# Kernel tuning notes

Measured on AMD Instinct MI355X. Metric: run time of the kernel, lower is better.

The kernel has to match this reference:

```python
import jax, jax.numpy as jnp
import numpy as np

B, H, W, C = 32, 256, 256, 3
FLAT = (H // 4) * (W // 4) * 64  # 64*64*64 = 262144 after two stride-2 SAME convs


def _conv(x, k, b, stride):
    y = jax.lax.conv_general_dilated(
        x, k, (stride, stride), 'SAME',
        dimension_numbers=('NHWC', 'HWIO', 'NHWC'))
    return jax.nn.relu(y + b)


def _grid_sample(img, theta):
    # STN: build normalized affine grid from theta [B,2,3], bilinear sample with
    # zero padding for out-of-bounds (GridSampler2D semantics).
    b, h, w, c = img.shape
    xs = (2.0 * jnp.arange(w, dtype=img.dtype) + 1.0) / w - 1.0
    ys = (2.0 * jnp.arange(h, dtype=img.dtype) + 1.0) / h - 1.0
    X, Y = jnp.meshgrid(xs, ys)                      # [H,W]
    base = jnp.stack([X, Y, jnp.ones_like(X)], -1)   # [H,W,3]
    g = jnp.einsum('bij,hwj->bhwi', theta, base)     # [B,H,W,2] (x,y) in [-1,1]
    px = (g[..., 0] + 1.0) * 0.5 * w - 0.5
    py = (g[..., 1] + 1.0) * 0.5 * h - 0.5
    x0 = jnp.floor(px); y0 = jnp.floor(py)
    wx1 = px - x0; wx0 = 1.0 - wx1
    wy1 = py - y0; wy0 = 1.0 - wy1

    bidx = jnp.arange(b)[:, None, None]

    def gather(yi, xi):
        valid = (xi >= 0) & (xi < w) & (yi >= 0) & (yi < h)
        xc = jnp.clip(xi, 0, w - 1).astype(jnp.int32)
        yc = jnp.clip(yi, 0, h - 1).astype(jnp.int32)
        v = img[bidx, yc, xc]                        # [B,H,W,C]
        return v * valid[..., None].astype(img.dtype)

    out = (gather(y0, x0) * (wy0 * wx0)[..., None]
           + gather(y0, x0 + 1) * (wy0 * wx1)[..., None]
           + gather(y0 + 1, x0) * (wy1 * wx0)[..., None]
           + gather(y0 + 1, x0 + 1) * (wy1 * wx1)[..., None])
    return out


def setup_inputs() -> dict:
    key = jax.random.key(0)
    ks = jax.random.split(key, 9)
    s = 0.05
    return {
        'inputs': jax.random.uniform(ks[0], (B, H, W, C), jnp.float32),
        'k1': jax.random.normal(ks[1], (3, 3, C, 32), jnp.float32) * s,
        'b1': jnp.zeros((32,), jnp.float32),
        'k2': jax.random.normal(ks[2], (3, 3, 32, 64), jnp.float32) * s,
        'b2': jnp.zeros((64,), jnp.float32),
        'w1': jax.random.normal(ks[3], (FLAT, 128), jnp.float32) * 0.002,
        'd1': jnp.zeros((128,), jnp.float32),
        'w2': jax.random.normal(ks[4], (128, 6), jnp.float32) * s,
        'd2': jnp.asarray([1, 0, 0, 0, 1, 0], jnp.float32),  # identity-ish bias
    }


def reference(inputs, k1, b1, k2, b2, w1, d1, w2, d2):
    x = _conv(inputs, k1, b1, 2)          # [B,H/2,W/2,32]
    x = _conv(x, k2, b2, 2)               # [B,H/4,W/4,64]
    x = x.reshape(x.shape[0], -1)         # [B,FLAT]
    x = jax.nn.relu(x @ w1 + d1)          # [B,128]
    theta = (x @ w2 + d2).reshape(-1, 2, 3)
    return _grid_sample(inputs, theta)
```

## Files before the change

### kernel.cpp

```cpp
#include <hip/hip_runtime.h>

#define IN_H 256
#define IN_W 256
#define C0   3
#define C1   32
#define H1   128
#define C2   64
#define H2   64
#define NB   32
#define K_FLAT (H2*H2*C2)
#define NHID 128

#define A1_IDX(b,p,y,ci,x2) ((((((size_t)(b)*2 + (p))*H1 + (y))*C1 + (ci))*64) + (x2))

__global__ __launch_bounds__(256, 8)
void conv1_k(const float* __restrict__ in, const float* __restrict__ k1,
             const float* __restrict__ b1, float* __restrict__ a1p) {
  __shared__ __align__(16) float rowL[3*IN_W*C0];
  const int tid = threadIdx.x;
  const int oy  = blockIdx.x;
  const int b   = blockIdx.y;

  {
    const float4* src = (const float4*)(in + (size_t)(b*IN_H + 2*oy)*IN_W*C0);
    float4* dst = (float4*)rowL;
    const float4 z = make_float4(0.f,0.f,0.f,0.f);
#pragma unroll
    for (int j = 0; j < 3; ++j) {
      const int i = tid + j*256;
      if (i < 3*IN_W*C0/4) {
        const int row = i / (IN_W*C0/4);
        const bool ok = (2*oy + row) < IN_H;
        dst[i] = ok ? src[i] : z;
      }
    }
  }
  __syncthreads();

  const int ox  = tid & 127;
  const int cg  = __builtin_amdgcn_readfirstlane((tid >> 7) * 16);

  float acc[16];
#pragma unroll
  for (int co = 0; co < 16; ++co) acc[co] = b1[cg + co];

#pragma unroll
  for (int dy = 0; dy < 3; ++dy) {
#pragma unroll
    for (int dx = 0; dx < 3; ++dx) {
      const int ix  = 2*ox + dx;
      const bool ok = ix < IN_W;
      const float m  = ok ? 1.f : 0.f;
      const int ixc = ok ? ix : (IN_W-1);
      const float* lp = rowL + (dy*IN_W + ixc)*C0;
      const float v0 = lp[0] * m;
      const float v1 = lp[1] * m;
      const float v2 = lp[2] * m;
      const float* wp = k1 + (size_t)((dy*3+dx)*C0)*C1 + cg;
#pragma unroll
      for (int co = 0; co < 16; ++co)
        acc[co] = fmaf(v0, wp[co],
                  fmaf(v1, wp[C1+co],
                  fmaf(v2, wp[2*C1+co], acc[co])));
    }
  }
  const int p  = ox & 1;
  const int x2 = ox >> 1;
#pragma unroll
  for (int co = 0; co < 16; ++co)
    a1p[A1_IDX(b, p, oy, cg + co, x2)] = fmaxf(acc[co], 0.f);
}

#define CONV2_DY_LOOP(EDGE_)                                                   \
  _Pragma("unroll")                                                            \
  for (int dy = 0; dy < 3; ++dy) {                                             \
    int iy = 2*oy + dy;                                                        \
    float rm = 1.f;                                                            \
    if (EDGE_) { if (iy >= H1) { iy = H1 - 1; rm = 0.f; } }                    \
    const float* r0 = a1p + A1_IDX(b, 0, iy, 0, 0) + 2*lx;                     \
    const float* r1 = a1p + A1_IDX(b, 1, iy, 0, 0) + 2*lx;                     \
    const float* wp = k2 + (size_t)(dy*3*C1)*C2 + cg16;                        \
    const float m2 = EDGE_ ? rm * xm : xm;                                     \
    _Pragma("unroll 8")                                                        \
    for (int ci = 0; ci < C1; ++ci) {                                          \
      const float2 Av = *(const float2*)(r0 + (size_t)ci*64);                  \
      const float  A2 = r0[(size_t)ci*64 + 2];                                 \
      const float2 Bv = *(const float2*)(r1 + (size_t)ci*64);                  \
      const float ax = EDGE_ ? Av.x*rm : Av.x;                                 \
      const float ay = EDGE_ ? Av.y*rm : Av.y;                                 \
      const float bx = EDGE_ ? Bv.x*rm : Bv.x;                                 \
      const float by = EDGE_ ? Bv.y*rm : Bv.y;                                 \
      const float a2v = A2 * m2;                                               \
      const float* w0  = wp + (size_t)ci*C2;                                   \
      const float* w1r = wp + (size_t)(C1 + ci)*C2;                            \
      const float* w2r = wp + (size_t)(2*C1 + ci)*C2;                          \
      _Pragma("unroll")                                                        \
      for (int co = 0; co < 16; ++co) {                                        \
        acc0[co] = fmaf(ax, w0[co],                                            \
                   fmaf(bx, w1r[co],                                           \
                   fmaf(ay,  w2r[co], acc0[co])));                             \
        acc1[co] = fmaf(ay, w0[co],                                            \
                   fmaf(by, w1r[co],                                           \
                   fmaf(a2v, w2r[co], acc1[co])));                             \
      }                                                                        \
    }                                                                          \
  }

__global__ __launch_bounds__(256, 4)
void conv2_k(const float* __restrict__ a1p, const float* __restrict__ k2,
             const float* __restrict__ b2, float* __restrict__ a2) {
  const int tid  = threadIdx.x;
  const int lane = tid & 63;
  const int lx   = lane & 31;
  const int oys  = lane >> 5;
  const int cg16 = __builtin_amdgcn_readfirstlane((tid >> 6) * 16);
  const int oy   = blockIdx.x * 2 + oys;
  const int b    = blockIdx.y;

  float acc0[16], acc1[16];
#pragma unroll
  for (int co = 0; co < 16; ++co) { acc0[co] = b2[cg16 + co]; acc1[co] = acc0[co]; }

  const float xm = (lx == 31) ? 0.f : 1.f;

  if (blockIdx.x == 31) {
    CONV2_DY_LOOP(1)
  } else {
    CONV2_DY_LOOP(0)
  }

  float* op = a2 + ((size_t)((b*H2 + oy)*H2) + 2*lx)*C2 + cg16;
#pragma unroll
  for (int g = 0; g < 4; ++g) {
    float4 o0;
    o0.x = fmaxf(acc0[4*g+0], 0.f);
    o0.y = fmaxf(acc0[4*g+1], 0.f);
    o0.z = fmaxf(acc0[4*g+2], 0.f);
    o0.w = fmaxf(acc0[4*g+3], 0.f);
    ((float4*)op)[g] = o0;
    float4 o1;
    o1.x = fmaxf(acc1[4*g+0], 0.f);
    o1.y = fmaxf(acc1[4*g+1], 0.f);
    o1.z = fmaxf(acc1[4*g+2], 0.f);
    o1.w = fmaxf(acc1[4*g+3], 0.f);
    ((float4*)(op + C2))[g] = o1;
  }
}

#define FC1_G   2048
#define KSPAN   (K_FLAT / FC1_G)
#define SUB     64
#define GC1     16

__global__ __launch_bounds__(256, 3)
void fc1_partial_k(const float* __restrict__ a2, const float* __restrict__ w1,
                   float* __restrict__ partial) {
  __shared__ __align__(16) float wL[SUB*NHID];
  __shared__ __align__(16) float xT[SUB*36];
  const int tid = threadIdx.x;
  const int q   = tid & 31;
  const int bo  = tid >> 5;
  const int k0  = blockIdx.x * KSPAN;

  float4 a0 = make_float4(0.f,0.f,0.f,0.f), a1v = a0, a2v = a0, a3v = a0;

#pragma unroll
  for (int r = 0; r < KSPAN/SUB; ++r) {
    const int ks = k0 + r*SUB;
    if (r) __syncthreads();

    {
      const float4* wsrc = (const float4*)(w1 + (size_t)ks*NHID);
#pragma unroll
      for (int j = 0; j < 8; ++j)
        ((float4*)wL)[tid + j*256] = wsrc[tid + j*256];
    }
    {
      const int lb  = tid >> 3;
      const int lkq = tid & 7;
#pragma unroll
      for (int j = 0; j < 2; ++j) {
        const int k4 = lkq*4 + j*32;
        float4 t = *(const float4*)(a2 + (size_t)lb*K_FLAT + ks + k4);
        xT[(k4+0)*36 + lb] = t.x;
        xT[(k4+1)*36 + lb] = t.y;
        xT[(k4+2)*36 + lb] = t.z;
        xT[(k4+3)*36 + lb] = t.w;
      }
    }
    __syncthreads();

#pragma unroll 8
    for (int k = 0; k < SUB; ++k) {
      const float4 w4 = *(const float4*)(wL + k*NHID + 4*q);
      const float4 xb = *(const float4*)&xT[k*36 + 4*bo];
      a0.x = fmaf(xb.x, w4.x, a0.x); a0.y = fmaf(xb.x, w4.y, a0.y);
      a0.z = fmaf(xb.x, w4.z, a0.z); a0.w = fmaf(xb.x, w4.w, a0.w);
      a1v.x = fmaf(xb.y, w4.x, a1v.x); a1v.y = fmaf(xb.y, w4.y, a1v.y);
      a1v.z = fmaf(xb.y, w4.z, a1v.z); a1v.w = fmaf(xb.y, w4.w, a1v.w);
      a2v.x = fmaf(xb.z, w4.x, a2v.x); a2v.y = fmaf(xb.z, w4.y, a2v.y);
      a2v.z = fmaf(xb.z, w4.z, a2v.z); a2v.w = fmaf(xb.z, w4.w, a2v.w);
      a3v.x = fmaf(xb.w, w4.x, a3v.x); a3v.y = fmaf(xb.w, w4.y, a3v.y);
      a3v.z = fmaf(xb.w, w4.z, a3v.z); a3v.w = fmaf(xb.w, w4.w, a3v.w);
    }
  }

  float* pp = partial + (size_t)blockIdx.x*(NB*NHID) + 4*q;
  *(float4*)(pp + (4*bo+0)*NHID) = a0;
  *(float4*)(pp + (4*bo+1)*NHID) = a1v;
  *(float4*)(pp + (4*bo+2)*NHID) = a2v;
  *(float4*)(pp + (4*bo+3)*NHID) = a3v;
}

__global__ __launch_bounds__(128, 8)
void fc1_reduce1_k(const float* __restrict__ partial, float* __restrict__ partial2) {
  const int t  = blockIdx.x*128 + threadIdx.x;
  const int gc = blockIdx.y;
  float s = 0.f;
#pragma unroll 8
  for (int g = gc*(FC1_G/GC1); g < gc*(FC1_G/GC1) + (FC1_G/GC1); ++g)
    s += partial[(size_t)g*(NB*NHID) + t];
  partial2[(size_t)gc*(NB*NHID) + t] = s;
}

__global__ __launch_bounds__(256)
void fc1_reduce2_k(const float* __restrict__ partial2, const float* __restrict__ d1,
                   float* __restrict__ h) {
  const int t = blockIdx.x*256 + threadIdx.x;
  float s = 0.f;
#pragma unroll
  for (int gc = 0; gc < GC1; ++gc) s += partial2[(size_t)gc*(NB*NHID) + t];
  h[t] = fmaxf(s + d1[t & (NHID-1)], 0.f);
}

__global__ __launch_bounds__(192)
void theta_k(const float* __restrict__ h, const float* __restrict__ w2,
             const float* __restrict__ d2, float* __restrict__ theta) {
  const int t = threadIdx.x;
  if (t >= NB*6) return;
  const int b = t / 6, j = t % 6;
  float s0 = 0.f, s1 = 0.f, s2 = 0.f, s3 = 0.f;
  for (int n = 0; n < NHID; n += 4) {
    s0 = fmaf(h[b*NHID + n+0], w2[(n+0)*6 + j], s0);
    s1 = fmaf(h[b*NHID + n+1], w2[(n+1)*6 + j], s1);
    s2 = fmaf(h[b*NHID + n+2], w2[(n+2)*6 + j], s2);
    s3 = fmaf(h[b*NHID + n+3], w2[(n+3)*6 + j], s3);
  }
  theta[t] = (s0 + s1) + (s2 + s3) + d2[j];
}

__global__ __launch_bounds__(256)
void sample_k(const float* __restrict__ img, const float* __restrict__ theta,
              float* __restrict__ out) {
  const int x = threadIdx.x;
  const int y = blockIdx.x & (IN_H-1);
  const int b = blockIdx.x >> 8;
  const float* tp = theta + b*6;
  const float t0 = tp[0], t1 = tp[1], t2 = tp[2];
  const float t3 = tp[3], t4 = tp[4], t5 = tp[5];

  const float xs = (2.f*x + 1.f)*(1.f/IN_W) - 1.f;
  const float ys = (2.f*y + 1.f)*(1.f/IN_H) - 1.f;
  const float gx = fmaf(t0, xs, fmaf(t1, ys, t2));
  const float gy = fmaf(t3, xs, fmaf(t4, ys, t5));
  const float px = fmaf(gx + 1.f, 0.5f*IN_W, -0.5f);
  const float py = fmaf(gy + 1.f, 0.5f*IN_H, -0.5f);

  const float x0f = floorf(px), y0f = floorf(py);
  const int ix0 = (int)x0f, iy0 = (int)y0f;
  const float wx1 = px - x0f, wx0 = 1.f - wx1;
  const float wy1 = py - y0f, wy0 = 1.f - wy1;

  float r = 0.f, g = 0.f, bl = 0.f;
  const float* ib = img + (size_t)b*IN_H*IN_W*C0;

  auto tap = [&](int yi, int xi, float w) {
    const bool v = (xi >= 0) && (xi < IN_W) && (yi >= 0) && (yi < IN_H);
    const int xc = xi < 0 ? 0 : (xi > IN_W-1 ? IN_W-1 : xi);
    const int yc = yi < 0 ? 0 : (yi > IN_H-1 ? IN_H-1 : yi);
    const float* p = ib + ((size_t)yc*IN_W + xc)*C0;
    if (v) {
      r  = fmaf(w, p[0], r);
      g  = fmaf(w, p[1], g);
      bl = fmaf(w, p[2], bl);
    }
  };
  tap(iy0,   ix0,   wy0*wx0);
  tap(iy0,   ix0+1, wy0*wx1);
  tap(iy0+1, ix0,   wy1*wx0);
  tap(iy0+1, ix0+1, wy1*wx1);

  float* op = out + ((size_t)(b*IN_H + y)*IN_W + x)*C0;
  op[0] = r; op[1] = g; op[2] = bl;
}

extern "C" void kernel_launch(void* const* d_in, const int* in_sizes, int n_in,
                              void* d_out, int out_size, void* d_ws, size_t ws_size,
                              hipStream_t stream) {
  const float* in = (const float*)d_in[0];
  const float* k1 = (const float*)d_in[1];
  const float* b1 = (const float*)d_in[2];
  const float* k2 = (const float*)d_in[3];
  const float* b2 = (const float*)d_in[4];
  const float* w1 = (const float*)d_in[5];
  const float* d1 = (const float*)d_in[6];
  const float* w2 = (const float*)d_in[7];
  const float* d2 = (const float*)d_in[8];
  float* out = (float*)d_out;
  float* ws  = (float*)d_ws;

  float* a1p     = ws;
  float* a2      = ws + (size_t)16777216;
  float* partial = ws;
  float* part2   = ws + (size_t)8388608;
  float* h       = ws + (size_t)8454144;
  float* th      = ws + (size_t)8458240;

  hipLaunchKernelGGL(conv1_k,       dim3(128, 32), dim3(256), 0, stream, in, k1, b1, a1p);
  hipLaunchKernelGGL(conv2_k,       dim3(32, 32),  dim3(256), 0, stream, a1p, k2, b2, a2);
  hipLaunchKernelGGL(fc1_partial_k, dim3(FC1_G),   dim3(256), 0, stream, a2, w1, partial);
  hipLaunchKernelGGL(fc1_reduce1_k, dim3(32, GC1), dim3(128), 0, stream, partial, part2);
  hipLaunchKernelGGL(fc1_reduce2_k, dim3(16),      dim3(256), 0, stream, part2, d1, h);
  hipLaunchKernelGGL(theta_k,       dim3(1),       dim3(192), 0, stream, h, w2, d2, th);
  hipLaunchKernelGGL(sample_k,      dim3(NB*IN_H), dim3(256), 0, stream, in, th, out);
}
```

Before: 350.8 us.

## Register-block fc1 partial GEMM 8x8 per thread with split-K across waves

The fc1 partial kernel now gives each thread an 8x8 tile of batch×hidden outputs, where before it held 4x4 accumulators. The block's K sub-tile is split across its four waves, and the wave partials are then combined through LDS in a tree reduction. Weights are permuted as they are stored in LDS so each thread reads its eight contiguous columns with two float4 loads. The xT row stride is padded to 40. This cuts LDS reads per FMA, but it adds extra barriers and an in-block reduction, and the larger accumulator set raises register pressure.

```diff
diff --git a/kernel.cpp b/kernel.cpp
--- a/kernel.cpp
+++ b/kernel.cpp
@@ -150,19 +150,26 @@
 #define FC1_G   2048
 #define KSPAN   (K_FLAT / FC1_G)
 #define SUB     64
+#define XSTR    40
 #define GC1     16
 
 __global__ __launch_bounds__(256, 3)
 void fc1_partial_k(const float* __restrict__ a2, const float* __restrict__ w1,
                    float* __restrict__ partial) {
   __shared__ __align__(16) float wL[SUB*NHID];
-  __shared__ __align__(16) float xT[SUB*36];
-  const int tid = threadIdx.x;
-  const int q   = tid & 31;
-  const int bo  = tid >> 5;
-  const int k0  = blockIdx.x * KSPAN;
-
-  float4 a0 = make_float4(0.f,0.f,0.f,0.f), a1v = a0, a2v = a0, a3v = a0;
+  __shared__ __align__(16) float xT[SUB*XSTR];
+  const int tid  = threadIdx.x;
+  const int w    = tid >> 6;
+  const int lane = tid & 63;
+  const int nq   = lane & 15;
+  const int bq   = lane >> 4;
+  const int k0   = blockIdx.x * KSPAN;
+
+  float acc[8][8];
+#pragma unroll
+  for (int i = 0; i < 8; ++i)
+#pragma unroll
+    for (int j = 0; j < 8; ++j) acc[i][j] = 0.f;
 
 #pragma unroll
   for (int r = 0; r < KSPAN/SUB; ++r) {
@@ -172,8 +179,13 @@
     {
       const float4* wsrc = (const float4*)(w1 + (size_t)ks*NHID);
 #pragma unroll
-      for (int j = 0; j < 8; ++j)
-        ((float4*)wL)[tid + j*256] = wsrc[tid + j*256];
+      for (int j = 0; j < 8; ++j) {
+        const int i    = tid + j*256;
+        const int krow = i >> 5;
+        const int qsrc = i & 31;
+        const int qdst = (qsrc & 1) ? 16 + (qsrc >> 1) : (qsrc >> 1);
+        ((float4*)wL)[krow*32 + qdst] = wsrc[i];
+      }
     }
     {
       const int lb  = tid >> 3;
@@ -182,34 +194,72 @@
       for (int j = 0; j < 2; ++j) {
         const int k4 = lkq*4 + j*32;
         float4 t = *(const float4*)(a2 + (size_t)lb*K_FLAT + ks + k4);
-        xT[(k4+0)*36 + lb] = t.x;
-        xT[(k4+1)*36 + lb] = t.y;
-        xT[(k4+2)*36 + lb] = t.z;
-        xT[(k4+3)*36 + lb] = t.w;
+        xT[(k4+0)*XSTR + lb] = t.x;
+        xT[(k4+1)*XSTR + lb] = t.y;
+        xT[(k4+2)*XSTR + lb] = t.z;
+        xT[(k4+3)*XSTR + lb] = t.w;
       }
     }
     __syncthreads();
 
-#pragma unroll 8
-    for (int k = 0; k < SUB; ++k) {
-      const float4 w4 = *(const float4*)(wL + k*NHID + 4*q);
-      const float4 xb = *(const float4*)&xT[k*36 + 4*bo];
-      a0.x = fmaf(xb.x, w4.x, a0.x); a0.y = fmaf(xb.x, w4.y, a0.y);
-      a0.z = fmaf(xb.x, w4.z, a0.z); a0.w = fmaf(xb.x, w4.w, a0.w);
-      a1v.x = fmaf(xb.y, w4.x, a1v.x); a1v.y = fmaf(xb.y, w4.y, a1v.y);
-      a1v.z = fmaf(xb.y, w4.z, a1v.z); a1v.w = fmaf(xb.y, w4.w, a1v.w);
-      a2v.x = fmaf(xb.z, w4.x, a2v.x); a2v.y = fmaf(xb.z, w4.y, a2v.y);
-      a2v.z = fmaf(xb.z, w4.z, a2v.z); a2v.w = fmaf(xb.z, w4.w, a2v.w);
-      a3v.x = fmaf(xb.w, w4.x, a3v.x); a3v.y = fmaf(xb.w, w4.y, a3v.y);
-      a3v.z = fmaf(xb.w, w4.z, a3v.z); a3v.w = fmaf(xb.w, w4.w, a3v.w);
-    }
-  }
-
-  float* pp = partial + (size_t)blockIdx.x*(NB*NHID) + 4*q;
-  *(float4*)(pp + (4*bo+0)*NHID) = a0;
-  *(float4*)(pp + (4*bo+1)*NHID) = a1v;
-  *(float4*)(pp + (4*bo+2)*NHID) = a2v;
-  *(float4*)(pp + (4*bo+3)*NHID) = a3v;
+#pragma unroll 2
+    for (int kk = 0; kk < SUB/4; ++kk) {
+      const int k = w*(SUB/4) + kk;
+      const float4 wa = ((const float4*)wL)[k*32 + nq];
+      const float4 wb = ((const float4*)wL)[k*32 + 16 + nq];
+      const float4 xa = *(const float4*)&xT[k*XSTR + 8*bq];
+      const float4 xb4 = *(const float4*)&xT[k*XSTR + 8*bq + 4];
+      const float xv[8] = {xa.x, xa.y, xa.z, xa.w, xb4.x, xb4.y, xb4.z, xb4.w};
+      const float wv[8] = {wa.x, wa.y, wa.z, wa.w, wb.x, wb.y, wb.z, wb.w};
+#pragma unroll
+      for (int i = 0; i < 8; ++i)
+#pragma unroll
+        for (int j = 0; j < 8; ++j)
+          acc[i][j] = fmaf(xv[i], wv[j], acc[i][j]);
+    }
+  }
+
+  float* s0 = wL;
+  float* s1 = wL + 4096;
+  __syncthreads();
+  if (w == 1 || w == 3) {
+    float* s = (w == 1) ? s0 : s1;
+#pragma unroll
+    for (int i = 0; i < 8; ++i)
+#pragma unroll
+      for (int j = 0; j < 8; ++j) s[(i*8+j)*64 + lane] = acc[i][j];
+  }
+  __syncthreads();
+  if (w == 0 || w == 2) {
+    const float* s = (w == 0) ? s0 : s1;
+#pragma unroll
+    for (int i = 0; i < 8; ++i)
+#pragma unroll
+      for (int j = 0; j < 8; ++j) acc[i][j] += s[(i*8+j)*64 + lane];
+  }
+  __syncthreads();
+  if (w == 2) {
+#pragma unroll
+    for (int i = 0; i < 8; ++i)
+#pragma unroll
+      for (int j = 0; j < 8; ++j) s0[(i*8+j)*64 + lane] = acc[i][j];
+  }
+  __syncthreads();
+  if (w == 0) {
+#pragma unroll
+    for (int i = 0; i < 8; ++i)
+#pragma unroll
+      for (int j = 0; j < 8; ++j) acc[i][j] += s0[(i*8+j)*64 + lane];
+    float* pp = partial + (size_t)blockIdx.x*(NB*NHID);
+#pragma unroll
+    for (int i = 0; i < 8; ++i) {
+      float4 o0 = make_float4(acc[i][0], acc[i][1], acc[i][2], acc[i][3]);
+      float4 o1 = make_float4(acc[i][4], acc[i][5], acc[i][6], acc[i][7]);
+      float* row = pp + (size_t)(8*bq + i)*NHID + 8*nq;
+      *(float4*)(row)     = o0;
+      *(float4*)(row + 4) = o1;
+    }
+  }
 }
 
 __global__ __launch_bounds__(128, 8)
```

Result: no change. 349.6 us (-0.3%).
